# Performance work log

Hardware: AMD Instinct MI355X
Metric: run time of the kernel (lower is better)

Reference implementation:

```python
import jax, jax.numpy as jnp
import numpy as np

NUM_CLASSES = 21
IGNORE_INDEX = 0
BN_EPS = 1e-5
VAR_EPS = 1e-6
NORM_EPS = 1e-12


def _class_stats(feat, onehot, counts):
    # feat: (B, C, P)  onehot: (B, P, K)  counts: (B, K)
    sums = jnp.einsum('bcp,bpk->bkc', feat, onehot)          # (B, K, C)
    sumsq = jnp.einsum('bcp,bpk->bkc', feat * feat, onehot)  # (B, K, C)
    cnt = counts[:, :, None]
    cnt_safe = jnp.maximum(cnt, 1.0)
    mu = sums / cnt_safe
    # unbiased variance, matching torch .var(dim=1) default
    denom = jnp.maximum(cnt - 1.0, 1.0)
    var = (sumsq - cnt * mu * mu) / denom + VAR_EPS
    return mu, var


def _l2_normalize(x):
    # F.normalize(x, p=2, dim=1): x / max(||x||_2, eps)
    n = jnp.sqrt(jnp.sum(x * x, axis=1, keepdims=True))
    return x / jnp.maximum(n, NORM_EPS)


def _ppa_forward(s_feat, t_feat, gt, W_proj, gamma, beta):
    # proj_s: 1x1 conv (no bias) + BatchNorm2d (training-mode batch stats) + ReLU
    x = jnp.einsum('bchw,oc->bohw', s_feat, W_proj)
    m = x.mean(axis=(0, 2, 3), keepdims=True)
    v = x.var(axis=(0, 2, 3), keepdims=True)  # biased, as BN uses
    x = (x - m) / jnp.sqrt(v + BN_EPS)
    x = x * gamma[None, :, None, None] + beta[None, :, None, None]
    s = jnp.maximum(x, 0.0)

    t = jax.lax.stop_gradient(t_feat)  # t_feat.detach()
    s = _l2_normalize(s)
    t = _l2_normalize(t)

    mse_total = jnp.mean((s - t) ** 2)

    B, C, H, W = s.shape
    P = H * W
    s_flat = s.reshape(B, C, P)
    t_flat = t.reshape(B, C, P)
    mask_flat = gt.reshape(B, P)

    onehot = jax.nn.one_hot(mask_flat, NUM_CLASSES, dtype=s.dtype)  # (B, P, K)
    counts = onehot.sum(axis=1)                                      # (B, K)

    mu_s, var_s = _class_stats(s_flat, onehot, counts)
    mu_t, var_t = _class_stats(t_flat, onehot, counts)

    # class valid iff count > 1 and class != ignore_index (same for s and t)
    class_ids = jnp.arange(NUM_CLASSES)
    valid = (counts > 1.0) & (class_ids[None, :] != IGNORE_INDEX)    # (B, K)

    loss_mu = jnp.mean((mu_s - mu_t) ** 2, axis=-1)    # (B, K)
    loss_var = jnp.mean((var_s - var_t) ** 2, axis=-1)  # (B, K)
    mm = 0.5 * loss_mu + 0.5 * loss_var

    cnt = jnp.sum(valid.astype(s.dtype))
    loss = jnp.sum(jnp.where(valid, mm, 0.0)) / (cnt + 1e-7)
    return loss + 0.5 * mse_total


def setup_inputs() -> dict:
    key = jax.random.key(0)
    k1, k2, k3, k4 = jax.random.split(key, 4)
    B, H, W = 8, 128, 128
    s_feat = jax.random.normal(k1, (B, 320, H, W), dtype=jnp.float32)
    t_feat = jax.random.normal(k2, (B, 256, H, W), dtype=jnp.float32)
    gt = jax.random.randint(k3, (B, H, W), 0, NUM_CLASSES)
    W_proj = jax.random.normal(k4, (256, 320), dtype=jnp.float32) * 0.05
    gamma = jnp.ones((256,), dtype=jnp.float32)
    beta = jnp.zeros((256,), dtype=jnp.float32)
    return {"s_feat": s_feat, "t_feat": t_feat, "gt": gt,
            "W_proj": W_proj, "gamma": gamma, "beta": beta}


def reference(s_feat, t_feat, gt, W_proj, gamma, beta):
    return _ppa_forward(s_feat, t_feat, gt, W_proj, gamma, beta)
```

## Files before the change

### kernel.cpp

```cpp
#include <hip/hip_runtime.h>
#include <hip/hip_bf16.h>

typedef unsigned short u16;
typedef __attribute__((ext_vector_type(2))) unsigned short us2;
typedef __attribute__((ext_vector_type(4))) float          f32x4;
typedef __attribute__((ext_vector_type(8))) short          bf8;
typedef __attribute__((ext_vector_type(8))) unsigned short us8;
typedef __attribute__((ext_vector_type(4))) unsigned short us4;

#define BATCH 8
#define CIN   320
#define COUT  256
#define NPIX  16384
#define NCLS  21
#define KCLS  32
#define MTOT  (BATCH*NPIX)
#define SROW  320
#define TSTR  66

__device__ __forceinline__ float bf2f(u16 v){
    unsigned int u = ((unsigned int)v) << 16;
    float f; __builtin_memcpy(&f, &u, 4); return f;
}
__device__ __forceinline__ u16 f2bf(float f){
    __hip_bfloat16 h = __float2bfloat16(f);
    u16 r; __builtin_memcpy(&r, &h, 2); return r;
}

__global__ void k0_wcvt(const float* __restrict__ W, u16* __restrict__ Wbf, float* __restrict__ zbuf){
    int i4 = blockIdx.x * 256 + threadIdx.x;
    float4 v = reinterpret_cast<const float4*>(W)[i4];
    us4 o;
    o[0] = f2bf(v.x); o[1] = f2bf(v.y); o[2] = f2bf(v.z); o[3] = f2bf(v.w);
    reinterpret_cast<us4*>(Wbf)[i4] = o;
    if (blockIdx.x == 0){
        for (int i = threadIdx.x; i < 832; i += 256) zbuf[i] = 0.f;
    }
}

__global__ __launch_bounds__(256) void kt_strans(const float* __restrict__ in, u16* __restrict__ out){
    __shared__ float tile[64*65];
    const int t  = threadIdx.x;
    const int bid = blockIdx.x;
    const int pt = bid & 255;
    const int ct = (bid >> 8) % 5;
    const int b  = bid / (256*5);
    const float* src = in + ((size_t)b*CIN + ct*64)*NPIX + pt*64;
    #pragma unroll
    for (int it = 0; it < 4; it++){
        int f = it*256 + t;
        int i = f >> 4, c4 = f & 15;
        float4 v = *reinterpret_cast<const float4*>(src + (size_t)i*NPIX + c4*4);
        float* d = &tile[i*65 + c4*4];
        d[0]=v.x; d[1]=v.y; d[2]=v.z; d[3]=v.w;
    }
    __syncthreads();
    u16* dst = out + ((size_t)(b*NPIX + pt*64))*SROW + ct*64;
    #pragma unroll
    for (int it = 0; it < 2; it++){
        int f = it*256 + t;
        int p = f >> 3, c8 = f & 7;
        us8 o;
        #pragma unroll
        for (int j = 0; j < 8; j++) o[j] = f2bf(tile[(c8*8+j)*65 + p]);
        *reinterpret_cast<us8*>(dst + (size_t)p*SROW + c8*8) = o;
    }
}

__global__ __launch_bounds__(256, 2) void k1_mfma(u16* SX, const u16* __restrict__ Wbf,
                                                  float* __restrict__ bnsum, float* __restrict__ bnsumsq){
    __shared__ __align__(16) char sm[67584];
    __shared__ float bns[512];
    const int t = threadIdx.x;
    const int wid = t >> 6, l = t & 63;
    const size_t pblk = (size_t)blockIdx.x * 128;
    const int wm = (wid & 1) * 64;
    const int wn = (wid >> 1) * 128;
    bns[t] = 0.f; bns[t+256] = 0.f;

    f32x4 acc[4][8];
    #pragma unroll
    for (int mi = 0; mi < 4; mi++)
        #pragma unroll
        for (int ni = 0; ni < 8; ni++)
            acc[mi][ni] = (f32x4){0.f,0.f,0.f,0.f};

    const int sg = t & 7, sp = t >> 3;
    const u16* srcb = SX + (pblk + sp) * SROW + sg * 8;
    us8 stg[4];
    #pragma unroll
    for (int it = 0; it < 4; it++)
        stg[it] = *reinterpret_cast<const us8*>(srcb + (size_t)it*32*SROW);

    for (int kt = 0; kt < 5; kt++){
        __syncthreads();
        #pragma unroll
        for (int it = 0; it < 4; it++){
            int p = sp + it*32;
            int byt = p*128 + ((sg*16) ^ ((p&7)<<4));
            *reinterpret_cast<us8*>(&sm[byt]) = stg[it];
        }
        if (kt < 4){
            #pragma unroll
            for (int it = 0; it < 4; it++)
                stg[it] = *reinterpret_cast<const us8*>(srcb + (size_t)it*32*SROW + (kt+1)*64);
        }
        __syncthreads();
        #pragma unroll
        for (int ks = 0; ks < 2; ks++){
            bf8 bfr[8], afr[4];
            const u16* wp = Wbf + (size_t)(wn + (l & 15)) * CIN + kt*64 + ks*32 + (l >> 4)*8;
            #pragma unroll
            for (int ni = 0; ni < 8; ni++)
                bfr[ni] = *reinterpret_cast<const bf8*>(wp + (size_t)ni*16*CIN);
            #pragma unroll
            for (int mi = 0; mi < 4; mi++){
                int p = wm + mi*16 + (l & 15);
                int byt = p*128 + (((ks*4 + (l>>4))*16) ^ ((p&7)<<4));
                afr[mi] = *reinterpret_cast<const bf8*>(&sm[byt]);
            }
            #pragma unroll
            for (int mi = 0; mi < 4; mi++)
                #pragma unroll
                for (int ni = 0; ni < 8; ni++)
                    acc[mi][ni] = __builtin_amdgcn_mfma_f32_16x16x32_bf16(afr[mi], bfr[ni], acc[mi][ni], 0, 0, 0);
        }
    }
    __syncthreads();
    #pragma unroll
    for (int mi = 0; mi < 4; mi++)
        #pragma unroll
        for (int ni = 0; ni < 8; ni++)
            #pragma unroll
            for (int r = 0; r < 4; r++){
                int p = wm + mi*16 + (l>>4)*4 + r;
                int o = wn + ni*16 + (l&15);
                *reinterpret_cast<u16*>(&sm[(p*264 + o)*2]) = f2bf(acc[mi][ni][r]);
            }
    __syncthreads();
    float s1[8], s2[8];
    #pragma unroll
    for (int j = 0; j < 8; j++){ s1[j] = 0.f; s2[j] = 0.f; }
    const int oc = (t & 31) * 8;
    const int pr = t >> 5;
    #pragma unroll
    for (int it = 0; it < 16; it++){
        int p = pr + it*8;
        us8 v = *reinterpret_cast<const us8*>(&sm[(p*264 + oc)*2]);
        *reinterpret_cast<us8*>(SX + (pblk + p)*SROW + oc) = v;
        #pragma unroll
        for (int j = 0; j < 8; j++){
            float fv = bf2f(v[j]);
            s1[j] += fv; s2[j] += fv*fv;
        }
    }
    #pragma unroll
    for (int j = 0; j < 8; j++){
        atomicAdd(&bns[oc + j],       s1[j]);
        atomicAdd(&bns[256 + oc + j], s2[j]);
    }
    __syncthreads();
    atomicAdd(&bnsum[t],   bns[t]);
    atomicAdd(&bnsumsq[t], bns[t + 256]);
}

__global__ void k3_counts(const int* __restrict__ gt, float* __restrict__ counts){
    __shared__ float h[NCLS];
    const int b = blockIdx.x >> 5, seg = blockIdx.x & 31, t = threadIdx.x;
    if (t < NCLS) h[t] = 0.f;
    __syncthreads();
    const int* g = gt + b * NPIX + seg * 512;
    for (int i = t; i < 512; i += 256) atomicAdd(&h[g[i]], 1.0f);
    __syncthreads();
    if (t < NCLS) atomicAdd(&counts[b * NCLS + t], h[t]);
}

__global__ __launch_bounds__(512, 2) void k4_fused(u16* SX, const float* __restrict__ T,
                                                   const int* __restrict__ gt,
                                                   const float* __restrict__ bnsum, const float* __restrict__ bnsumsq,
                                                   const float* __restrict__ gamma, const float* __restrict__ beta,
                                                   float* __restrict__ msep){
    __shared__ u16 sbb[256*TSTR];
    __shared__ float nt_l[64];
    __shared__ float rt_l[64];
    __shared__ int   gtile[64];
    __shared__ float msw[8];
    const int t = threadIdx.x, wid = t >> 6, l = t & 63;
    const int b  = blockIdx.x >> 6;
    const int pb = (blockIdx.x & 63) * 256;
    const float inv = 1.0f / (float)MTOT;
    float a0, a1, a2, a3, c0, c1, c2, c3;
    {
        float m0 = bnsum[l      ]*inv, v0 = bnsumsq[l      ]*inv - m0*m0;
        float m1 = bnsum[l + 64 ]*inv, v1 = bnsumsq[l + 64 ]*inv - m1*m1;
        float m2 = bnsum[l + 128]*inv, v2 = bnsumsq[l + 128]*inv - m2*m2;
        float m3 = bnsum[l + 192]*inv, v3 = bnsumsq[l + 192]*inv - m3*m3;
        a0 = gamma[l      ] / sqrtf(v0 + 1e-5f); c0 = beta[l      ] - m0*a0;
        a1 = gamma[l + 64 ] / sqrtf(v1 + 1e-5f); c1 = beta[l + 64 ] - m1*a1;
        a2 = gamma[l + 128] / sqrtf(v2 + 1e-5f); c2 = beta[l + 128] - m2*a2;
        a3 = gamma[l + 192] / sqrtf(v3 + 1e-5f); c3 = beta[l + 192] - m3*a3;
    }
    const float* Tb = T + (size_t)b * COUT * NPIX;
    const int* gtb = gt + b * NPIX;
    const u16* Xb = SX + (size_t)b * NPIX * SROW;
    float msea = 0.f;

    f32x4 acc[4][2][2];
    #pragma unroll
    for (int ty = 0; ty < 4; ty++)
        #pragma unroll
        for (int sl = 0; sl < 2; sl++)
            #pragma unroll
            for (int hf = 0; hf < 2; hf++)
                acc[ty][sl][hf] = (f32x4){0.f,0.f,0.f,0.f};

    const int sc4 = t >> 4, sp4 = t & 15;
    f32x4 pstg[8];
    int gstg = 0;
    {
        #pragma unroll
        for (int it = 0; it < 8; it++)
            pstg[it] = *reinterpret_cast<const f32x4*>(Tb + (size_t)(it*32 + sc4)*NPIX + pb + sp4*4);
        if (t < 64) gstg = gtb[pb + t];
    }

    for (int tile = 0; tile < 4; tile++){
        const int q0 = pb + tile*64;
        if (t < 64) nt_l[t] = 0.f;
        __syncthreads();
        {
            float nq0=0.f, nq1=0.f, nq2=0.f, nq3=0.f;
            #pragma unroll
            for (int it = 0; it < 8; it++){
                f32x4 v = pstg[it];
                nq0 += v[0]*v[0]; nq1 += v[1]*v[1]; nq2 += v[2]*v[2]; nq3 += v[3]*v[3];
            }
            atomicAdd(&nt_l[sp4*4+0], nq0);
            atomicAdd(&nt_l[sp4*4+1], nq1);
            atomicAdd(&nt_l[sp4*4+2], nq2);
            atomicAdd(&nt_l[sp4*4+3], nq3);
            if (t < 64) gtile[t] = gstg;
        }
        if (tile < 3){
            const int q1 = q0 + 64;
            #pragma unroll
            for (int it = 0; it < 8; it++)
                pstg[it] = *reinterpret_cast<const f32x4*>(Tb + (size_t)(it*32 + sc4)*NPIX + q1 + sp4*4);
            if (t < 64) gstg = gtb[q1 + t];
        }
        __syncthreads();
        if (t < 64) rt_l[t] = 1.0f / fmaxf(sqrtf(nt_l[t]), 1e-12f);
        #pragma unroll
        for (int u = 0; u < 8; u++){
            int pxl = wid*8 + u;
            const u16* xr = Xb + (size_t)(q0 + pxl) * SROW;
            float s0 = fmaxf(fmaf(a0, bf2f(xr[l]),     c0), 0.f);
            float s1 = fmaxf(fmaf(a1, bf2f(xr[l+64]),  c1), 0.f);
            float s2 = fmaxf(fmaf(a2, bf2f(xr[l+128]), c2), 0.f);
            float s3 = fmaxf(fmaf(a3, bf2f(xr[l+192]), c3), 0.f);
            float ns = s0*s0 + s1*s1 + s2*s2 + s3*s3;
            #pragma unroll
            for (int off = 32; off; off >>= 1) ns += __shfl_xor(ns, off, 64);
            float rs = 1.0f / fmaxf(sqrtf(ns), 1e-12f);
            sbb[(l      )*TSTR + pxl] = f2bf(s0*rs);
            sbb[(l + 64 )*TSTR + pxl] = f2bf(s1*rs);
            sbb[(l + 128)*TSTR + pxl] = f2bf(s2*rs);
            sbb[(l + 192)*TSTR + pxl] = f2bf(s3*rs);
        }
        __syncthreads();
        #pragma unroll
        for (int ks = 0; ks < 2; ks++){
            const int px0 = ks*32 + (l>>4)*8;
            bf8 aA0, aA1;
            #pragma unroll
            for (int j = 0; j < 8; j++){
                int gv = gtile[px0 + j];
                aA0[j] = (short)((gv == (l & 15))      ? 0x3F80 : 0);
                aA1[j] = (short)((gv == (l & 15) + 16) ? 0x3F80 : 0);
            }
            float rtj[8];
            #pragma unroll
            for (int q = 0; q < 4; q++){
                float2 rv = *reinterpret_cast<const float2*>(&rt_l[px0 + 2*q]);
                rtj[2*q] = rv.x; rtj[2*q+1] = rv.y;
            }
            #pragma unroll
            for (int sl = 0; sl < 2; sl++){
                const int cw = wid*16 + (l & 15) + sl*128;
                const float* tg = Tb + (size_t)cw*NPIX + q0 + px0;
                f32x4 ta = *reinterpret_cast<const f32x4*>(tg);
                f32x4 tb4 = *reinterpret_cast<const f32x4*>(tg + 4);
                const int sbase = cw*TSTR + px0;
                bf8 bS, bS2, bT, bT2;
                #pragma unroll
                for (int q = 0; q < 4; q++){
                    us2 sv = *reinterpret_cast<const us2*>(&sbb[sbase + 2*q]);
                    #pragma unroll
                    for (int e = 0; e < 2; e++){
                        int j = 2*q + e;
                        float traw = (j < 4) ? ta[j] : tb4[j-4];
                        float ft = traw * rtj[j];
                        float fs = bf2f(sv[e]);
                        bT[j]  = (short)f2bf(ft);
                        bT2[j] = (short)f2bf(ft*ft);
                        bS[j]  = (short)sv[e];
                        bS2[j] = (short)f2bf(fs*fs);
                        float d = fs - ft;
                        msea += d*d;
                    }
                }
                acc[0][sl][0] = __builtin_amdgcn_mfma_f32_16x16x32_bf16(aA0, bS,  acc[0][sl][0], 0,0,0);
                acc[0][sl][1] = __builtin_amdgcn_mfma_f32_16x16x32_bf16(aA1, bS,  acc[0][sl][1], 0,0,0);
                acc[1][sl][0] = __builtin_amdgcn_mfma_f32_16x16x32_bf16(aA0, bS2, acc[1][sl][0], 0,0,0);
                acc[1][sl][1] = __builtin_amdgcn_mfma_f32_16x16x32_bf16(aA1, bS2, acc[1][sl][1], 0,0,0);
                acc[2][sl][0] = __builtin_amdgcn_mfma_f32_16x16x32_bf16(aA0, bT,  acc[2][sl][0], 0,0,0);
                acc[2][sl][1] = __builtin_amdgcn_mfma_f32_16x16x32_bf16(aA1, bT,  acc[2][sl][1], 0,0,0);
                acc[3][sl][0] = __builtin_amdgcn_mfma_f32_16x16x32_bf16(aA0, bT2, acc[3][sl][0], 0,0,0);
                acc[3][sl][1] = __builtin_amdgcn_mfma_f32_16x16x32_bf16(aA1, bT2, acc[3][sl][1], 0,0,0);
            }
        }
    }

    {
        u16* Pb = SX + (size_t)blockIdx.x * 256 * SROW;
        #pragma unroll
        for (int ty = 0; ty < 4; ty++)
            #pragma unroll
            for (int sl = 0; sl < 2; sl++)
                #pragma unroll
                for (int hf = 0; hf < 2; hf++)
                    #pragma unroll
                    for (int r = 0; r < 4; r++){
                        int k = hf*16 + (l>>4)*4 + r;
                        int c = wid*16 + (l & 15) + sl*128;
                        int i = (ty*KCLS + k)*COUT + c;
                        Pb[(size_t)(i >> 7)*SROW + (i & 127)] = f2bf(acc[ty][sl][hf][r]);
                    }
    }
    #pragma unroll
    for (int off = 32; off; off >>= 1) msea += __shfl_xor(msea, off, 64);
    if (l == 0) msw[wid] = msea;
    __syncthreads();
    if (t == 0){
        float v = 0.f;
        #pragma unroll
        for (int i = 0; i < 8; i++) v += msw[i];
        atomicAdd(msep, v);
    }
}

__global__ void kR_reduce(const u16* __restrict__ SX,
                          float* __restrict__ gss, float* __restrict__ gsq,
                          float* __restrict__ gts, float* __restrict__ gtq){
    int g = blockIdx.x * 256 + threadIdx.x;
    #pragma unroll
    for (int it = 0; it < 4; it++, g += 65536){
        int i  = g & 32767;
        int b  = g >> 15;
        float s = 0.f;
        #pragma unroll
        for (int sl = 0; sl < 64; sl++){
            const u16* p = SX + ((size_t)((b*64 + sl)*256 + (i >> 7)))*SROW + (i & 127);
            s += bf2f(*p);
        }
        int ty = i >> 13;
        int kc = i & 8191;
        float* G = (ty==0)? gss : (ty==1)? gsq : (ty==2)? gts : gtq;
        G[b*8192 + kc] = s;
    }
}

__global__ void kA_pairs(const float* __restrict__ counts,
                         const float* __restrict__ gs,  const float* __restrict__ gqs,
                         const float* __restrict__ gtm, const float* __restrict__ gqt,
                         float* __restrict__ mmacc, float* __restrict__ ccacc){
    __shared__ float red[4];
    const int bk = blockIdx.x;
    const int b = bk / NCLS, k = bk - b*NCLS;
    const int t = threadIdx.x, wid = t >> 6, l = t & 63;
    const float cnt = counts[bk];
    const float cs = fmaxf(cnt, 1.f);
    const float dn = fmaxf(cnt - 1.f, 1.f);
    const int idx = (b*KCLS + k)*COUT + t;
    float mus = gs[idx] / cs;
    float vas = (gqs[idx] - cnt*mus*mus) / dn + 1e-6f;
    float mut = gtm[idx] / cs;
    float vat = (gqt[idx] - cnt*mut*mut) / dn + 1e-6f;
    float dm = mus - mut, dv = vas - vat;
    float a = dm*dm + dv*dv;
    #pragma unroll
    for (int off = 32; off; off >>= 1) a += __shfl_xor(a, off, 64);
    if (l == 0) red[wid] = a;
    __syncthreads();
    if (t == 0 && cnt > 1.f && k != 0){
        atomicAdd(mmacc, 0.5f * (red[0]+red[1]+red[2]+red[3]) / (float)COUT);
        atomicAdd(ccacc, 1.f);
    }
}

__global__ void kB_final(const float* __restrict__ mmacc, const float* __restrict__ ccacc,
                         const float* __restrict__ msep, float* __restrict__ out){
    out[0] = mmacc[0] / (ccacc[0] + 1e-7f) + 0.5f * (msep[0] / (float)((size_t)MTOT * COUT));
}

extern "C" void kernel_launch(void* const* d_in, const int* in_sizes, int n_in,
                              void* d_out, int out_size, void* d_ws, size_t ws_size,
                              hipStream_t stream){
    (void)in_sizes; (void)n_in; (void)out_size; (void)ws_size;
    const float* s_feat = (const float*)d_in[0];
    const float* t_feat = (const float*)d_in[1];
    const int*   gt     = (const int*)d_in[2];
    const float* Wp     = (const float*)d_in[3];
    const float* gamma  = (const float*)d_in[4];
    const float* beta   = (const float*)d_in[5];
    char* ws = (char*)d_ws;

    u16*   SX   = (u16*)ws;
    u16*   Wbf  = (u16*)(ws + 83886080);
    char*  z0   = ws + 84049920;
    float* bnsum    = (float*)(z0);
    float* bnsumsq  = (float*)(z0 + 1024);
    float* msep     = (float*)(z0 + 2048);
    float* mmacc    = (float*)(z0 + 2064);
    float* ccacc    = (float*)(z0 + 2080);
    float* counts   = (float*)(z0 + 2304);
    float* gsum_s   = (float*)(z0 + 5376);
    float* gsumsq_s = (float*)(z0 + 5376 + 262144);
    float* gsum_t   = (float*)(z0 + 5376 + 2*262144);
    float* gsumsq_t = (float*)(z0 + 5376 + 3*262144);


    k0_wcvt  <<<80,    256, 0, stream>>>(Wp, Wbf, (float*)z0);
    kt_strans<<<10240, 256, 0, stream>>>(s_feat, SX);
    k1_mfma  <<<1024,  256, 0, stream>>>(SX, Wbf, bnsum, bnsumsq);
    k3_counts<<<256,   256, 0, stream>>>(gt, counts);
    k4_fused <<<512,   512, 0, stream>>>(SX, t_feat, gt, bnsum, bnsumsq, gamma, beta, msep);
    kR_reduce<<<256,   256, 0, stream>>>(SX, gsum_s, gsumsq_s, gsum_t, gsumsq_t);
    kA_pairs <<<168,   256, 0, stream>>>(counts, gsum_s, gsumsq_s, gsum_t, gsumsq_t, mmacc, ccacc);
    kB_final <<<1,     1,   0, stream>>>(mmacc, ccacc, msep, (float*)d_out);
}
```

Measured before the change: 227.2 us.

## Widen transpose tiles and fuse partial-sum reduction into class-pair kernel

```diff
diff --git a/kernel.cpp b/kernel.cpp
--- a/kernel.cpp
+++ b/kernel.cpp
@@ -38,31 +38,30 @@
     }
 }
 
-__global__ __launch_bounds__(256) void kt_strans(const float* __restrict__ in, u16* __restrict__ out){
-    __shared__ float tile[64*65];
-    const int t  = threadIdx.x;
+__global__ __launch_bounds__(512) void kt_strans(const float* __restrict__ in, u16* __restrict__ out){
+    __shared__ float tile[64*257];
+    const int t = threadIdx.x, lane = t & 63, wv = t >> 6;
     const int bid = blockIdx.x;
-    const int pt = bid & 255;
-    const int ct = (bid >> 8) % 5;
-    const int b  = bid / (256*5);
-    const float* src = in + ((size_t)b*CIN + ct*64)*NPIX + pt*64;
+    const int pt = bid & 63;
+    const int ct = (bid >> 6) % 5;
+    const int b  = bid / 320;
+    const float* src = in + ((size_t)b*CIN + ct*64)*NPIX + pt*256;
+    #pragma unroll
+    for (int it = 0; it < 8; it++){
+        int r = it*8 + wv;
+        f32x4 v = *reinterpret_cast<const f32x4*>(src + (size_t)r*NPIX + lane*4);
+        float* d = &tile[r*257 + lane*4];
+        d[0]=v[0]; d[1]=v[1]; d[2]=v[2]; d[3]=v[3];
+    }
+    __syncthreads();
+    u16* dst = out + ((size_t)(b*NPIX + pt*256))*SROW + ct*64;
     #pragma unroll
     for (int it = 0; it < 4; it++){
-        int f = it*256 + t;
-        int i = f >> 4, c4 = f & 15;
-        float4 v = *reinterpret_cast<const float4*>(src + (size_t)i*NPIX + c4*4);
-        float* d = &tile[i*65 + c4*4];
-        d[0]=v.x; d[1]=v.y; d[2]=v.z; d[3]=v.w;
-    }
-    __syncthreads();
-    u16* dst = out + ((size_t)(b*NPIX + pt*64))*SROW + ct*64;
-    #pragma unroll
-    for (int it = 0; it < 2; it++){
-        int f = it*256 + t;
+        int f = it*512 + t;
         int p = f >> 3, c8 = f & 7;
         us8 o;
         #pragma unroll
-        for (int j = 0; j < 8; j++) o[j] = f2bf(tile[(c8*8+j)*65 + p]);
+        for (int j = 0; j < 8; j++) o[j] = f2bf(tile[(c8*8+j)*257 + p]);
         *reinterpret_cast<us8*>(dst + (size_t)p*SROW + c8*8) = o;
     }
 }
@@ -349,43 +348,29 @@
     }
 }
 
-__global__ void kR_reduce(const u16* __restrict__ SX,
-                          float* __restrict__ gss, float* __restrict__ gsq,
-                          float* __restrict__ gts, float* __restrict__ gtq){
-    int g = blockIdx.x * 256 + threadIdx.x;
-    #pragma unroll
-    for (int it = 0; it < 4; it++, g += 65536){
-        int i  = g & 32767;
-        int b  = g >> 15;
-        float s = 0.f;
-        #pragma unroll
-        for (int sl = 0; sl < 64; sl++){
-            const u16* p = SX + ((size_t)((b*64 + sl)*256 + (i >> 7)))*SROW + (i & 127);
-            s += bf2f(*p);
-        }
-        int ty = i >> 13;
-        int kc = i & 8191;
-        float* G = (ty==0)? gss : (ty==1)? gsq : (ty==2)? gts : gtq;
-        G[b*8192 + kc] = s;
-    }
-}
-
-__global__ void kA_pairs(const float* __restrict__ counts,
-                         const float* __restrict__ gs,  const float* __restrict__ gqs,
-                         const float* __restrict__ gtm, const float* __restrict__ gqt,
-                         float* __restrict__ mmacc, float* __restrict__ ccacc){
+__global__ void kRA_pairs(const u16* __restrict__ SX, const float* __restrict__ counts,
+                          float* __restrict__ mmacc, float* __restrict__ ccacc){
     __shared__ float red[4];
     const int bk = blockIdx.x;
     const int b = bk / NCLS, k = bk - b*NCLS;
     const int t = threadIdx.x, wid = t >> 6, l = t & 63;
+    float sums[4];
+    #pragma unroll
+    for (int ty = 0; ty < 4; ty++){
+        int i = (ty*KCLS + k)*COUT + t;
+        const u16* p = SX + ((size_t)(b*64)*256 + (i >> 7))*SROW + (i & 127);
+        float s = 0.f;
+        #pragma unroll
+        for (int sl = 0; sl < 64; sl++) s += bf2f(p[(size_t)sl * 256 * SROW]);
+        sums[ty] = s;
+    }
     const float cnt = counts[bk];
     const float cs = fmaxf(cnt, 1.f);
     const float dn = fmaxf(cnt - 1.f, 1.f);
-    const int idx = (b*KCLS + k)*COUT + t;
-    float mus = gs[idx] / cs;
-    float vas = (gqs[idx] - cnt*mus*mus) / dn + 1e-6f;
-    float mut = gtm[idx] / cs;
-    float vat = (gqt[idx] - cnt*mut*mut) / dn + 1e-6f;
+    float mus = sums[0] / cs;
+    float vas = (sums[1] - cnt*mus*mus) / dn + 1e-6f;
+    float mut = sums[2] / cs;
+    float vat = (sums[3] - cnt*mut*mut) / dn + 1e-6f;
     float dm = mus - mut, dv = vas - vat;
     float a = dm*dm + dv*dv;
     #pragma unroll
@@ -424,18 +409,13 @@
     float* mmacc    = (float*)(z0 + 2064);
     float* ccacc    = (float*)(z0 + 2080);
     float* counts   = (float*)(z0 + 2304);
-    float* gsum_s   = (float*)(z0 + 5376);
-    float* gsumsq_s = (float*)(z0 + 5376 + 262144);
-    float* gsum_t   = (float*)(z0 + 5376 + 2*262144);
-    float* gsumsq_t = (float*)(z0 + 5376 + 3*262144);
 
 
     k0_wcvt  <<<80,    256, 0, stream>>>(Wp, Wbf, (float*)z0);
-    kt_strans<<<10240, 256, 0, stream>>>(s_feat, SX);
+    kt_strans<<<2560,  512, 0, stream>>>(s_feat, SX);
     k1_mfma  <<<1024,  256, 0, stream>>>(SX, Wbf, bnsum, bnsumsq);
     k3_counts<<<256,   256, 0, stream>>>(gt, counts);
     k4_fused <<<512,   512, 0, stream>>>(SX, t_feat, gt, bnsum, bnsumsq, gamma, beta, msep);
-    kR_reduce<<<256,   256, 0, stream>>>(SX, gsum_s, gsumsq_s, gsum_t, gsumsq_t);
-    kA_pairs <<<168,   256, 0, stream>>>(counts, gsum_s, gsumsq_s, gsum_t, gsumsq_t, mmacc, ccacc);
+    kRA_pairs<<<168,   256, 0, stream>>>(SX, counts, mmacc, ccacc);
     kB_final <<<1,     1,   0, stream>>>(mmacc, ccacc, msep, (float*)d_out);
 }
```

After: 286.9 us. 26.3% more time.
